# Optimization experiments

Measured on AMD Instinct MI355X. Metric: run time of the kernel, lower is better.

The kernel has to match this reference:

```python
import jax, jax.numpy as jnp
import numpy as np

H = 32        # num_heads
E = 128       # hidden_dim (per-head K/V/query dim)
D_STATE = 512 # encoder state width
B, LQ, LK = 8, 1024, 1024


def setup_inputs() -> dict:
    key = jax.random.key(0)
    ks = jax.random.split(key, 8)
    query = jax.random.normal(ks[0], (B, LQ, E), dtype=jnp.float32)
    states = jax.random.normal(ks[1], (B, LK, D_STATE), dtype=jnp.float32)
    s = 1.0 / np.sqrt(D_STATE)
    Wk = jax.random.uniform(ks[2], (H, D_STATE, E), minval=-s, maxval=s, dtype=jnp.float32)
    bk = jax.random.uniform(ks[3], (H, E), minval=-s, maxval=s, dtype=jnp.float32)
    Wv = jax.random.uniform(ks[4], (H, D_STATE, E), minval=-s, maxval=s, dtype=jnp.float32)
    bv = jax.random.uniform(ks[5], (H, E), minval=-s, maxval=s, dtype=jnp.float32)
    so = 1.0 / np.sqrt(H * E)
    Wo = jax.random.uniform(ks[6], (H * E, E), minval=-so, maxval=so, dtype=jnp.float32)
    bo = jax.random.uniform(ks[7], (E,), minval=-so, maxval=so, dtype=jnp.float32)
    return {"query": query, "states": states, "Wk": Wk, "bk": bk,
            "Wv": Wv, "bv": bv, "Wo": Wo, "bo": bo}


def reference(query, states, Wk, bk, Wv, bv, Wo, bo):
    # Per-head K/V projections of the shared states: [H,B,Lk,E]
    keys = jnp.einsum('bkd,hde->hbke', states, Wk) + bk[:, None, None, :]
    values = jnp.einsum('bkd,hde->hbke', states, Wv) + bv[:, None, None, :]
    # Scaled dot-product scores: [H,B,Lq,Lk]
    scale = 1.0 / jnp.sqrt(jnp.asarray(E, dtype=query.dtype))
    scores = jnp.einsum('bqe,hbke->hbqk', query, keys) * scale
    # Original detaches the softmax output before AV
    attn = jax.lax.stop_gradient(jax.nn.softmax(scores, axis=-1))
    ctx = jnp.einsum('hbqk,hbke->hbqe', attn, values)       # [H,B,Lq,E]
    # concat heads along last dim: [B,Lq,H*E]
    ctx = jnp.transpose(ctx, (1, 2, 0, 3)).reshape(query.shape[0], query.shape[1], -1)
    return ctx @ Wo + bo
```

## Files before the change

kernel.cpp:

```cpp
#include <hip/hip_runtime.h>

#define H_  32
#define E_  128
#define D_  512
#define B_  8
#define LQ_ 1024
#define LK_ 1024

typedef __bf16 bf16x8 __attribute__((ext_vector_type(8)));
typedef float  f32x4  __attribute__((ext_vector_type(4)));
typedef float  f32x16 __attribute__((ext_vector_type(16)));

typedef __attribute__((address_space(1))) const unsigned int guint;
typedef __attribute__((address_space(3))) unsigned int luint;

__device__ __forceinline__ f32x4 MFMA16(bf16x8 a, bf16x8 b, f32x4 c) {
    return __builtin_amdgcn_mfma_f32_16x16x32_bf16(a, b, c, 0, 0, 0);
}
__device__ __forceinline__ f32x16 MFMA32(bf16x8 a, bf16x8 b, f32x16 c) {
    return __builtin_amdgcn_mfma_f32_32x32x16_bf16(a, b, c, 0, 0, 0);
}

__device__ __forceinline__ unsigned short f2bf(float x) {
    union { float f; unsigned u; } v; v.f = x;
    unsigned r = v.u + 0x7fffu + ((v.u >> 16) & 1u);
    return (unsigned short)(r >> 16);
}
__device__ __forceinline__ unsigned pkbf(float a, float b) {
    union { float f; unsigned u; } x, y; x.f = a; y.f = b;
    return __builtin_amdgcn_perm(y.u, x.u, 0x07060302u);
}

__global__ void conv_scale_kernel(const float* __restrict__ in,
                                  unsigned short* __restrict__ out,
                                  long n4, float scale) {
    long i = blockIdx.x * (long)blockDim.x + threadIdx.x;
    long stride = (long)gridDim.x * blockDim.x;
    for (; i < n4; i += stride) {
        float4 v = ((const float4*)in)[i];
        union { unsigned long long u; unsigned short s[4]; } p;
        p.s[0] = f2bf(v.x * scale); p.s[1] = f2bf(v.y * scale);
        p.s[2] = f2bf(v.z * scale); p.s[3] = f2bf(v.w * scale);
        ((unsigned long long*)out)[i] = p.u;
    }
}

__global__ void transpose_bf16_kernel(const float* __restrict__ in,
                                      unsigned short* __restrict__ out,
                                      int R, int C, long inStride, long outStride) {
    in  += (long)blockIdx.z * inStride;
    out += (long)blockIdx.z * outStride;
    __shared__ float t[32][33];
    int x = threadIdx.x, y = threadIdx.y;
    int c0 = blockIdx.x * 32, r0 = blockIdx.y * 32;
    for (int i = 0; i < 32; i += 8) t[y + i][x] = in[(long)(r0 + y + i) * C + (c0 + x)];
    __syncthreads();
    for (int i = 0; i < 32; i += 8)
        out[(long)(c0 + y + i) * R + (r0 + x)] = f2bf(t[x][y + i]);
}

__global__ __launch_bounds__(512, 4) void kv_proj_kernel(
    const unsigned short* __restrict__ sb,
    const unsigned short* __restrict__ wkt,
    const unsigned short* __restrict__ wvt,
    const float* __restrict__ bk, const float* __restrict__ bv,
    unsigned short* __restrict__ Kb,
    unsigned short* __restrict__ Vtb)
{
    int bid = blockIdx.x;
    const int x = bid & 7;  int s = bid >> 3;
    const int mt = s & 3;   s >>= 2;
    const int b  = s & 7;   s >>= 3;
    const int kv = s & 1;   s >>= 1;
    const int h  = s * 8 + x;

    const unsigned short* wt = kv ? wvt : wkt;
    const float* bias = kv ? bv : bk;

    __shared__ unsigned short As[2][256 * 40];
    __shared__ unsigned short Bs[2][128 * 40];

    const int tid = threadIdx.x;
    const int wave = tid >> 6, lane = tid & 63;
    const int ln = lane & 31, hi = lane >> 5;
    const int wm = wave & 3, wn = wave >> 2;

    const unsigned short* Ag = sb + ((long)b * LK_ + mt * 256) * D_;
    const unsigned short* Bg = wt + (long)h * E_ * D_;

    uint4 ap[2], bp;
    #pragma unroll
    for (int p = 0; p < 2; p++) {
        int id = p * 512 + tid;
        ap[p] = *(const uint4*)&Ag[(long)(id >> 2) * D_ + (id & 3) * 8];
    }
    bp = *(const uint4*)&Bg[(long)(tid >> 2) * D_ + (tid & 3) * 8];
    #pragma unroll
    for (int p = 0; p < 2; p++) {
        int id = p * 512 + tid;
        *(uint4*)&As[0][(id >> 2) * 40 + (id & 3) * 8] = ap[p];
    }
    *(uint4*)&Bs[0][(tid >> 2) * 40 + (tid & 3) * 8] = bp;
    __syncthreads();

    f32x16 acc[4] = {};

    for (int it = 0; it < 16; it++) {
        const int buf = it & 1;
        if (it < 15) {
            const int d0 = (it + 1) * 32;
            #pragma unroll
            for (int p = 0; p < 2; p++) {
                int id = p * 512 + tid;
                ap[p] = *(const uint4*)&Ag[(long)(id >> 2) * D_ + d0 + (id & 3) * 8];
            }
            bp = *(const uint4*)&Bg[(long)(tid >> 2) * D_ + d0 + (tid & 3) * 8];
        }
        #pragma unroll
        for (int ss = 0; ss < 2; ss++) {
            const int ko = ss * 16 + hi * 8;
            bf16x8 af[2], bfr[2];
            #pragma unroll
            for (int mb = 0; mb < 2; mb++)
                af[mb] = *(const bf16x8*)&As[buf][(wm * 64 + mb * 32 + ln) * 40 + ko];
            #pragma unroll
            for (int nb = 0; nb < 2; nb++)
                bfr[nb] = *(const bf16x8*)&Bs[buf][(wn * 64 + nb * 32 + ln) * 40 + ko];
            #pragma unroll
            for (int mb = 0; mb < 2; mb++)
                #pragma unroll
                for (int nb = 0; nb < 2; nb++)
                    acc[mb * 2 + nb] = MFMA32(af[mb], bfr[nb], acc[mb * 2 + nb]);
        }
        if (it < 15) {
            #pragma unroll
            for (int p = 0; p < 2; p++) {
                int id = p * 512 + tid;
                *(uint4*)&As[buf ^ 1][(id >> 2) * 40 + (id & 3) * 8] = ap[p];
            }
            *(uint4*)&Bs[buf ^ 1][(tid >> 2) * 40 + (tid & 3) * 8] = bp;
            __syncthreads();
        }
    }

    const int row0 = mt * 256 + wm * 64;
    const int e0 = wn * 64;
    if (!kv) {
        const long base = ((long)h * B_ + b) * LK_;
        #pragma unroll
        for (int mb = 0; mb < 2; mb++)
            #pragma unroll
            for (int nb = 0; nb < 2; nb++) {
                const int e = e0 + nb * 32 + ln;
                const float be = bias[h * E_ + e];
                #pragma unroll
                for (int r = 0; r < 16; r++) {
                    int row = row0 + mb * 32 + (r & 3) + 8 * (r >> 2) + 4 * hi;
                    Kb[(base + row) * E_ + e] = f2bf(acc[mb * 2 + nb][r] + be);
                }
            }
    } else {
        const long vbase = ((long)h * B_ + b) * E_;
        #pragma unroll
        for (int mb = 0; mb < 2; mb++)
            #pragma unroll
            for (int nb = 0; nb < 2; nb++) {
                const int e = e0 + nb * 32 + ln;
                const float be = bias[h * E_ + e];
                #pragma unroll
                for (int rg = 0; rg < 4; rg++) {
                    int k0 = row0 + mb * 32 + 8 * rg + 4 * hi;
                    union { unsigned long long u; unsigned short s2[4]; } pk;
                    #pragma unroll
                    for (int j = 0; j < 4; j++)
                        pk.s2[j] = f2bf(acc[mb * 2 + nb][rg * 4 + j] + be);
                    *(unsigned long long*)&Vtb[(vbase + e) * (long)LK_ + k0] = pk.u;
                }
            }
    }
}

__global__ __launch_bounds__(256, 2) void attn_kernel(
    const unsigned short* __restrict__ qb,
    const unsigned short* __restrict__ Kb,
    const unsigned short* __restrict__ Vtb,
    unsigned short* __restrict__ ctx)
{
    int bid = blockIdx.x;
    const int b = bid & 7;
    int s = bid >> 3;
    const int qt = s & 7;
    const int h  = s >> 3;

    __shared__ unsigned short Ks[2][64 * 128];
    __shared__ unsigned short Vs[2][128 * 64];

    const int tid = threadIdx.x;
    const int wave = tid >> 6, lane = tid & 63;
    const int ln = lane & 31, hi = lane >> 5;

    const unsigned short* Kg = Kb  + ((long)h * B_ + b) * (long)LK_ * E_;
    const unsigned short* Vg = Vtb + ((long)h * B_ + b) * (long)E_ * LK_;
    const int qrow = qt * 128 + wave * 32;

    bf16x8 qf[8];
    #pragma unroll
    for (int s8 = 0; s8 < 8; s8++) {
        union { uint4 u; bf16x8 v; } t;
        t.u = *(const uint4*)&qb[((long)b * LQ_ + qrow + ln) * E_ + s8 * 16 + hi * 8];
        qf[s8] = t.v;
    }

    int koff[4], voff[4];
    #pragma unroll
    for (int d = 0; d < 4; d++) {
        int krow = (wave * 4 + d) * 4 + (lane >> 4);
        int kc = (lane & 15) ^ (krow & 15);
        koff[d] = krow * E_ + kc * 8;
        int vrow = (wave * 4 + d) * 8 + (lane >> 3);
        int vc = (lane & 7) ^ (vrow & 7);
        voff[d] = vrow * LK_ + vc * 8;
    }

    #define STAGE(t_, buf_)                                                         \
        do {                                                                        \
            _Pragma("unroll")                                                       \
            for (int d = 0; d < 4; d++) {                                           \
                __builtin_amdgcn_global_load_lds(                                   \
                    (guint*)(Kg + (long)(t_) * (64 * E_) + koff[d]),                \
                    (luint*)&Ks[buf_][(wave * 4 + d) * 512], 16, 0, 0);             \
                __builtin_amdgcn_global_load_lds(                                   \
                    (guint*)(Vg + (t_) * 64 + voff[d]),                             \
                    (luint*)&Vs[buf_][(wave * 4 + d) * 512], 16, 0, 0);             \
            }                                                                       \
        } while (0)

    STAGE(0, 0);
    __syncthreads();

    f32x16 O[4] = {};
    float l_run = 0.f;

    for (int t = 0; t < 16; t++) {
        const int buf = t & 1;
        if (t < 15) STAGE(t + 1, buf ^ 1);

        f32x16 S[2] = {};
        #pragma unroll
        for (int es = 0; es < 8; es++) {
            #pragma unroll
            for (int mb = 0; mb < 2; mb++) {
                const int row = mb * 32 + ln;
                const int cs = (es * 2 + hi) ^ (row & 15);
                bf16x8 kf = *(const bf16x8*)&Ks[buf][row * 128 + cs * 8];
                S[mb] = MFMA32(kf, qf[es], S[mb]);
            }
        }

        float tsum = 0.f;
        #pragma unroll
        for (int mb = 0; mb < 2; mb++) {
            float pv[16];
            #pragma unroll
            for (int r = 0; r < 16; r++) {
                pv[r] = __builtin_amdgcn_exp2f(S[mb][r]);
                tsum += pv[r];
            }
            unsigned a0 = pkbf(pv[0],  pv[1]),  b0 = pkbf(pv[2],  pv[3]);
            unsigned a1 = pkbf(pv[4],  pv[5]),  b1 = pkbf(pv[6],  pv[7]);
            unsigned a2 = pkbf(pv[8],  pv[9]),  b2 = pkbf(pv[10], pv[11]);
            unsigned a3 = pkbf(pv[12], pv[13]), b3 = pkbf(pv[14], pv[15]);
            unsigned r0 = __shfl_xor(hi ? a0 : a1, 32, 64);
            unsigned r1 = __shfl_xor(hi ? b0 : b1, 32, 64);
            unsigned r2 = __shfl_xor(hi ? a2 : a3, 32, 64);
            unsigned r3 = __shfl_xor(hi ? b2 : b3, 32, 64);
            #pragma unroll
            for (int st = 0; st < 2; st++) {
                union { unsigned u[4]; bf16x8 v; } pa;
                if (st == 0) {
                    pa.u[0] = hi ? r0 : a0;  pa.u[1] = hi ? r1 : b0;
                    pa.u[2] = hi ? a1 : r0;  pa.u[3] = hi ? b1 : r1;
                } else {
                    pa.u[0] = hi ? r2 : a2;  pa.u[1] = hi ? r3 : b2;
                    pa.u[2] = hi ? a3 : r2;  pa.u[3] = hi ? b3 : r3;
                }
                #pragma unroll
                for (int nb = 0; nb < 4; nb++) {
                    const int vrow = nb * 32 + ln;
                    const int vc = (mb * 4 + st * 2 + hi) ^ (vrow & 7);
                    bf16x8 vf = *(const bf16x8*)&Vs[buf][vrow * 64 + vc * 8];
                    O[nb] = MFMA32(pa.v, vf, O[nb]);
                }
            }
        }
        tsum += __shfl_xor(tsum, 32, 64);
        l_run += tsum;

        __syncthreads();
    }

    const float linv = 1.f / l_run;
    #pragma unroll
    for (int r = 0; r < 16; r++) {
        const int rowmap = (r & 3) + 8 * (r >> 2) + 4 * hi;
        float lv = __shfl(linv, rowmap, 64);
        int qg = qrow + rowmap;
        long rowbase = ((long)b * LQ_ + qg) * (H_ * E_) + h * E_;
        #pragma unroll
        for (int nb = 0; nb < 4; nb++)
            ctx[rowbase + nb * 32 + ln] = f2bf(O[nb][r] * lv);
    }
}

__global__ void init_out_kernel(float* __restrict__ out, const float* __restrict__ bo) {
    int i = blockIdx.x * blockDim.x + threadIdx.x;
    float4 b4 = ((const float4*)bo)[i & 31];
    ((float4*)out)[i] = b4;
}

__global__ __launch_bounds__(256) void out_proj_kernel(
    const unsigned short* __restrict__ ctx,
    const unsigned short* __restrict__ wot,
    float* __restrict__ out)
{
    const int qt = blockIdx.x;
    const int kc = blockIdx.y;
    __shared__ unsigned short As[128 * 72];
    __shared__ unsigned short Bs[128 * 72];
    const int tid = threadIdx.x;
    const int wave = tid >> 6, lane = tid & 63;
    const int lq = lane & 15, quad = lane >> 4;
    const long kbase = (long)kc * 1024;

    f32x4 acc[2][8] = {};

    for (int d0 = 0; d0 < 1024; d0 += 64) {
        __syncthreads();
        for (int i = 0; i < 4; i++) {
            int g = i * 256 + tid;
            int row = g >> 3, cc = (g & 7) * 8;
            *(uint4*)&As[row * 72 + cc] =
                *(const uint4*)&ctx[(long)(qt * 128 + row) * (H_ * E_) + kbase + d0 + cc];
            *(uint4*)&Bs[row * 72 + cc] =
                *(const uint4*)&wot[(long)row * (H_ * E_) + kbase + d0 + cc];
        }
        __syncthreads();
        for (int ds = 0; ds < 64; ds += 32) {
            bf16x8 a0 = *(const bf16x8*)&As[(wave * 32 + lq) * 72 + ds + quad * 8];
            bf16x8 a1 = *(const bf16x8*)&As[(wave * 32 + 16 + lq) * 72 + ds + quad * 8];
            for (int et = 0; et < 8; et++) {
                bf16x8 bb = *(const bf16x8*)&Bs[(et * 16 + lq) * 72 + ds + quad * 8];
                acc[0][et] = MFMA16(a0, bb, acc[0][et]);
                acc[1][et] = MFMA16(a1, bb, acc[1][et]);
            }
        }
    }
    for (int kt = 0; kt < 2; kt++)
        for (int et = 0; et < 8; et++)
            for (int r = 0; r < 4; r++) {
                int q = qt * 128 + wave * 32 + kt * 16 + quad * 4 + r;
                int eo = et * 16 + lq;
                atomicAdd(&out[(long)q * E_ + eo], acc[kt][et][r]);
            }
}

extern "C" void kernel_launch(void* const* d_in, const int* in_sizes, int n_in,
                              void* d_out, int out_size, void* d_ws, size_t ws_size,
                              hipStream_t stream) {
    const float* query  = (const float*)d_in[0];
    const float* states = (const float*)d_in[1];
    const float* Wk     = (const float*)d_in[2];
    const float* bk     = (const float*)d_in[3];
    const float* Wv     = (const float*)d_in[4];
    const float* bv     = (const float*)d_in[5];
    const float* Wo     = (const float*)d_in[6];
    const float* bo     = (const float*)d_in[7];
    float* out = (float*)d_out;

    const size_t WS_QB  = 0;
    const size_t WS_SB  = WS_QB  + 2097152UL;
    const size_t WS_WKT = WS_SB  + 8388608UL;
    const size_t WS_WVT = WS_WKT + 4194304UL;
    const size_t WS_WOT = WS_WVT + 4194304UL;
    const size_t WS_KB  = WS_WOT + 1048576UL;
    const size_t WS_VTB = WS_KB  + 67108864UL;
    const size_t WS_CTX = WS_VTB + 67108864UL;
    const size_t WS_END = WS_CTX + 67108864UL;
    if (ws_size < WS_END) return;

    char* ws = (char*)d_ws;
    unsigned short* qb  = (unsigned short*)(ws + WS_QB);
    unsigned short* sb  = (unsigned short*)(ws + WS_SB);
    unsigned short* wkt = (unsigned short*)(ws + WS_WKT);
    unsigned short* wvt = (unsigned short*)(ws + WS_WVT);
    unsigned short* wot = (unsigned short*)(ws + WS_WOT);
    unsigned short* Kb  = (unsigned short*)(ws + WS_KB);
    unsigned short* Vtb = (unsigned short*)(ws + WS_VTB);
    unsigned short* ctx = (unsigned short*)(ws + WS_CTX);

    const float SCALE = 0.12751744f;

    conv_scale_kernel<<<512, 256, 0, stream>>>(query, qb, (long)(B_ * LQ_ * E_ / 4), SCALE);
    conv_scale_kernel<<<1024, 256, 0, stream>>>(states, sb, (long)(B_ * LK_ * D_ / 4), 1.0f);
    transpose_bf16_kernel<<<dim3(4, 16, 32), dim3(32, 8), 0, stream>>>(
        Wk, wkt, D_, E_, (long)D_ * E_, (long)D_ * E_);
    transpose_bf16_kernel<<<dim3(4, 16, 32), dim3(32, 8), 0, stream>>>(
        Wv, wvt, D_, E_, (long)D_ * E_, (long)D_ * E_);
    transpose_bf16_kernel<<<dim3(4, 128, 1), dim3(32, 8), 0, stream>>>(
        Wo, wot, H_ * E_, E_, 0L, 0L);

    kv_proj_kernel<<<2048, 512, 0, stream>>>(sb, wkt, wvt, bk, bv, Kb, Vtb);
    attn_kernel<<<2048, 256, 0, stream>>>(qb, Kb, Vtb, ctx);

    init_out_kernel<<<1024, 256, 0, stream>>>(out, bo);
    out_proj_kernel<<<dim3(64, 4), 256, 0, stream>>>(ctx, wot, out);
}
```

Measured before the change: 380.5 us.

## Store V in MFMA-packed layout, load directly to registers, split out-proj reduction

The V projection now writes values in a packed layout that matches the PV MFMA operand, so the attention kernel loads V fragments straight from global memory into registers and no longer stages them through LDS. The LDS use per block is roughly halved and the occupancy hint is dropped. The output projection now splits K into 8 chunks that write partial sums, followed by a separate reduce kernel that adds the bias, replacing the atomicAdd accumulation. The kv_proj block-index decode and its launch bounds also change. Direct global V loads give up LDS reuse and can add latency and redundant global traffic.

```diff
diff --git a/kernel.cpp b/kernel.cpp
--- a/kernel.cpp
+++ b/kernel.cpp
@@ -59,7 +59,7 @@
         out[(long)(c0 + y + i) * R + (r0 + x)] = f2bf(t[x][y + i]);
 }
 
-__global__ __launch_bounds__(512, 4) void kv_proj_kernel(
+__global__ __launch_bounds__(512, 2) void kv_proj_kernel(
     const unsigned short* __restrict__ sb,
     const unsigned short* __restrict__ wkt,
     const unsigned short* __restrict__ wvt,
@@ -69,9 +69,9 @@
 {
     int bid = blockIdx.x;
     const int x = bid & 7;  int s = bid >> 3;
+    const int kv = s & 1;   s >>= 1;
     const int mt = s & 3;   s >>= 2;
     const int b  = s & 7;   s >>= 3;
-    const int kv = s & 1;   s >>= 1;
     const int h  = s * 8 + x;
 
     const unsigned short* wt = kv ? wvt : wkt;
@@ -160,7 +160,7 @@
                 }
             }
     } else {
-        const long vbase = ((long)h * B_ + b) * E_;
+        const long vbase = ((long)h * B_ + b) * (long)E_ * LK_;
         #pragma unroll
         for (int mb = 0; mb < 2; mb++)
             #pragma unroll
@@ -174,13 +174,13 @@
                     #pragma unroll
                     for (int j = 0; j < 4; j++)
                         pk.s2[j] = f2bf(acc[mb * 2 + nb][rg * 4 + j] + be);
-                    *(unsigned long long*)&Vtb[(vbase + e) * (long)LK_ + k0] = pk.u;
+                    *(unsigned long long*)&Vtb[vbase + ((long)(k0 >> 3) * E_ + e) * 8 + 4 * hi] = pk.u;
                 }
             }
     }
 }
 
-__global__ __launch_bounds__(256, 2) void attn_kernel(
+__global__ __launch_bounds__(256) void attn_kernel(
     const unsigned short* __restrict__ qb,
     const unsigned short* __restrict__ Kb,
     const unsigned short* __restrict__ Vtb,
@@ -193,7 +193,6 @@
     const int h  = s >> 3;
 
     __shared__ unsigned short Ks[2][64 * 128];
-    __shared__ unsigned short Vs[2][128 * 64];
 
     const int tid = threadIdx.x;
     const int wave = tid >> 6, lane = tid & 63;
@@ -211,15 +210,12 @@
         qf[s8] = t.v;
     }
 
-    int koff[4], voff[4];
+    int koff[4];
     #pragma unroll
     for (int d = 0; d < 4; d++) {
         int krow = (wave * 4 + d) * 4 + (lane >> 4);
         int kc = (lane & 15) ^ (krow & 15);
         koff[d] = krow * E_ + kc * 8;
-        int vrow = (wave * 4 + d) * 8 + (lane >> 3);
-        int vc = (lane & 7) ^ (vrow & 7);
-        voff[d] = vrow * LK_ + vc * 8;
     }
 
     #define STAGE(t_, buf_)                                                         \
@@ -229,9 +225,6 @@
                 __builtin_amdgcn_global_load_lds(                                   \
                     (guint*)(Kg + (long)(t_) * (64 * E_) + koff[d]),                \
                     (luint*)&Ks[buf_][(wave * 4 + d) * 512], 16, 0, 0);             \
-                __builtin_amdgcn_global_load_lds(                                   \
-                    (guint*)(Vg + (t_) * 64 + voff[d]),                             \
-                    (luint*)&Vs[buf_][(wave * 4 + d) * 512], 16, 0, 0);             \
             }                                                                       \
         } while (0)
 
@@ -260,6 +253,14 @@
         float tsum = 0.f;
         #pragma unroll
         for (int mb = 0; mb < 2; mb++) {
+            union { uint4 u; bf16x8 v; } vf[2][4];
+            #pragma unroll
+            for (int st = 0; st < 2; st++) {
+                const long kpack = (long)t * 8 + mb * 4 + st * 2 + hi;
+                #pragma unroll
+                for (int nb = 0; nb < 4; nb++)
+                    vf[st][nb].u = *(const uint4*)&Vg[(kpack * E_ + nb * 32 + ln) * 8];
+            }
             float pv[16];
             #pragma unroll
             for (int r = 0; r < 16; r++) {
@@ -285,12 +286,8 @@
                     pa.u[2] = hi ? a3 : r2;  pa.u[3] = hi ? b3 : r3;
                 }
                 #pragma unroll
-                for (int nb = 0; nb < 4; nb++) {
-                    const int vrow = nb * 32 + ln;
-                    const int vc = (mb * 4 + st * 2 + hi) ^ (vrow & 7);
-                    bf16x8 vf = *(const bf16x8*)&Vs[buf][vrow * 64 + vc * 8];
-                    O[nb] = MFMA32(pa.v, vf, O[nb]);
-                }
+                for (int nb = 0; nb < 4; nb++)
+                    O[nb] = MFMA32(pa.v, vf[st][nb].v, O[nb]);
             }
         }
         tsum += __shfl_xor(tsum, 32, 64);
@@ -312,16 +309,10 @@
     }
 }
 
-__global__ void init_out_kernel(float* __restrict__ out, const float* __restrict__ bo) {
-    int i = blockIdx.x * blockDim.x + threadIdx.x;
-    float4 b4 = ((const float4*)bo)[i & 31];
-    ((float4*)out)[i] = b4;
-}
-
-__global__ __launch_bounds__(256) void out_proj_kernel(
+__global__ __launch_bounds__(256) void out_proj_part_kernel(
     const unsigned short* __restrict__ ctx,
     const unsigned short* __restrict__ wot,
-    float* __restrict__ out)
+    float* __restrict__ part)
 {
     const int qt = blockIdx.x;
     const int kc = blockIdx.y;
@@ -330,11 +321,11 @@
     const int tid = threadIdx.x;
     const int wave = tid >> 6, lane = tid & 63;
     const int lq = lane & 15, quad = lane >> 4;
-    const long kbase = (long)kc * 1024;
+    const long kbase = (long)kc * 512;
 
     f32x4 acc[2][8] = {};
 
-    for (int d0 = 0; d0 < 1024; d0 += 64) {
+    for (int d0 = 0; d0 < 512; d0 += 64) {
         __syncthreads();
         for (int i = 0; i < 4; i++) {
             int g = i * 256 + tid;
@@ -355,13 +346,27 @@
             }
         }
     }
+    float* pout = part + (long)kc * (B_ * LQ_ * E_);
     for (int kt = 0; kt < 2; kt++)
         for (int et = 0; et < 8; et++)
             for (int r = 0; r < 4; r++) {
                 int q = qt * 128 + wave * 32 + kt * 16 + quad * 4 + r;
                 int eo = et * 16 + lq;
-                atomicAdd(&out[(long)q * E_ + eo], acc[kt][et][r]);
-            }
+                pout[(long)q * E_ + eo] = acc[kt][et][r];
+            }
+}
+
+__global__ void out_reduce_kernel(const float* __restrict__ part,
+                                  const float* __restrict__ bo,
+                                  float* __restrict__ out) {
+    int i = blockIdx.x * blockDim.x + threadIdx.x;
+    float4 s = ((const float4*)bo)[i & 31];
+    #pragma unroll
+    for (int kc = 0; kc < 8; kc++) {
+        float4 p = ((const float4*)part)[(long)kc * 262144 + i];
+        s.x += p.x; s.y += p.y; s.z += p.z; s.w += p.w;
+    }
+    ((float4*)out)[i] = s;
 }
 
 extern "C" void kernel_launch(void* const* d_in, const int* in_sizes, int n_in,
@@ -397,6 +402,7 @@
     unsigned short* Kb  = (unsigned short*)(ws + WS_KB);
     unsigned short* Vtb = (unsigned short*)(ws + WS_VTB);
     unsigned short* ctx = (unsigned short*)(ws + WS_CTX);
+    float* part = (float*)(ws + WS_KB);
 
     const float SCALE = 0.12751744f;
 
@@ -412,6 +418,6 @@
     kv_proj_kernel<<<2048, 512, 0, stream>>>(sb, wkt, wvt, bk, bv, Kb, Vtb);
     attn_kernel<<<2048, 256, 0, stream>>>(qb, Kb, Vtb, ctx);
 
-    init_out_kernel<<<1024, 256, 0, stream>>>(out, bo);
-    out_proj_kernel<<<dim3(64, 4), 256, 0, stream>>>(ctx, wot, out);
-}
+    out_proj_part_kernel<<<dim3(64, 8), 256, 0, stream>>>(ctx, wot, part);
+    out_reduce_kernel<<<1024, 256, 0, stream>>>(part, bo, out);
+}
```

Measured after the change: 452.9 us. 1.19x slower.
